# Kernel optimization log

Hardware: AMD Instinct MI355X
Metric: run time of the kernel (lower is better)

## Reference

```python
import jax, jax.numpy as jnp
import numpy as np
import math

N_NODES, N_EDGES = 10000, 160000
CS, CZ, CH, NH, PQ, PV = 384, 128, 192, 12, 4, 8
INF, EPS = 100000.0, 1e-8


def setup_inputs() -> dict:
    key = jax.random.key(0)
    ks = iter(jax.random.split(key, 48))

    def rn(shape, scale=1.0):
        return jax.random.normal(next(ks), shape, jnp.float32) * scale

    def lin(din, dout):
        return rn((din, dout), 1.0 / math.sqrt(din)), jnp.zeros((dout,), jnp.float32)

    s = rn((N_NODES, CS))
    z = rn((N_EDGES, CZ))
    edge_index = jax.random.randint(next(ks), (2, N_EDGES), 0, N_NODES)
    # proper random rotations via QR (sign-corrected)
    A = rn((N_NODES, 3, 3))
    Q, R = jnp.linalg.qr(A)
    rots = Q * jnp.sign(jnp.diagonal(R, axis1=-2, axis2=-1))[:, None, :]
    trans = rn((N_NODES, 3), 10.0)
    mask = jnp.ones((N_NODES,), jnp.float32)
    Ww1, bw1 = lin(2 * CS + CZ, CH)
    Ww2, bw2 = lin(CH, CH)
    Ww3, bw3 = lin(CH, NH)
    Wv1, bv1 = lin(CS + CZ, CH)
    Wv2, bv2 = lin(CH, CH)
    Wv3, bv3 = lin(CH, CH)
    Wq, bq = lin(CS, NH * PQ * 3)
    Wkv, bkv = lin(CS, NH * (PQ + PV) * 3)
    Wb, bb = lin(CZ, NH)
    Wdz, bdz = lin(CZ, CZ // 4)
    Wo, bo = lin(NH * (CZ // 4 + CH // NH + PV * 4), CS)
    hw = jnp.full((NH,), math.log(math.e - 1.0), jnp.float32)  # softplus^-1(1)
    return dict(s=s, z=z, edge_index=edge_index, rots=rots, trans=trans, mask=mask,
                Ww1=Ww1, bw1=bw1, Ww2=Ww2, bw2=bw2, Ww3=Ww3, bw3=bw3,
                Wv1=Wv1, bv1=bv1, Wv2=Wv2, bv2=bv2, Wv3=Wv3, bv3=bv3,
                Wq=Wq, bq=bq, Wkv=Wkv, bkv=bkv, Wb=Wb, bb=bb,
                Wdz=Wdz, bdz=bdz, Wo=Wo, bo=bo, hw=hw)


def _points(flat, rots, t, P):
    # flat [N, 3P] is coord-major (split into 3 chunks then stacked last): p[n, p, c] = flat[n, c*P + p]
    p = flat.reshape(flat.shape[0], 3, P).transpose(0, 2, 1)
    return jnp.einsum('nij,npj->npi', rots, p) + t[:, None, :]


def _forward(s, z, edge_index, rots, trans, mask,
             Ww1, bw1, Ww2, bw2, Ww3, bw3,
             Wv1, bv1, Wv2, bv2, Wv3, bv3,
             Wq, bq, Wkv, bkv, Wb, bb, Wdz, bdz, Wo, bo, hw):
    n = s.shape[0]
    src = edge_index[1]
    dst = edge_index[0]
    t = trans * 0.1  # r.scale_translation(1/10)
    q_pts = _points(s @ Wq + bq, rots, t, NH * PQ).reshape(n, NH, PQ, 3)
    kv_pts = _points(s @ Wkv + bkv, rots, t, NH * (PQ + PV)).reshape(n, NH, PQ + PV, 3)
    k_pts, v_pts = kv_pts[:, :, :PQ], kv_pts[:, :, PQ:]
    b = z @ Wb + bb  # [E, NH]
    w_ins = jnp.concatenate([s[src], s[dst], z], axis=-1)  # [E, 2*CS+CZ]
    h = jax.nn.relu(w_ins @ Ww1 + bw1)
    h = jax.nn.relu(h @ Ww2 + bw2)
    a = (h @ Ww3 + bw3) * math.sqrt(1.0 / (3 * CH)) + math.sqrt(1.0 / 3) * b
    disp = q_pts[src] - k_pts[dst]  # [E, NH, PQ, 3]
    pt_att = jnp.sum(disp ** 2, axis=-1)  # [E, NH, PQ]
    hw_sp = jax.nn.softplus(hw)[None, :, None] * math.sqrt(1.0 / (3 * (PQ * 9.0 / 2)))
    pt_att = jnp.sum(pt_att * hw_sp, axis=-1) * (-0.5)  # [E, NH]
    edge_mask = INF * (mask[dst] * mask[src] - 1.0)
    a = a + pt_att + edge_mask[:, None]
    # segment softmax grouped by edge_index[1]
    amax = jax.ops.segment_max(a, src, num_segments=n)
    ex = jnp.exp(a - amax[src])
    denom = jax.ops.segment_sum(ex, src, num_segments=n)
    a = ex / (denom[src] + 1e-16)
    v_in = jnp.concatenate([s[dst], z], axis=-1)
    h = jax.nn.relu(v_in @ Wv1 + bv1)
    h = jax.nn.relu(h @ Wv2 + bv2)
    v_dst = (h @ Wv3 + bv3).reshape(-1, NH, CH // NH)
    o = jax.ops.segment_sum(a[..., None] * v_dst, src, num_segments=n).reshape(n, -1)
    o_pt = jax.ops.segment_sum(a[..., None, None] * v_pts[dst], src, num_segments=n)  # [n, NH, PV, 3]
    o_pt = jnp.einsum('nji,nhpj->nhpi', rots, o_pt - t[:, None, None, :])  # invert_apply: R^T (x - t)
    o_pt_norm = jnp.sqrt(jnp.sum(o_pt ** 2, axis=-1) + EPS).reshape(n, -1)
    o_pt_flat = o_pt.reshape(n, NH * PV, 3)
    pair_z = z @ Wdz + bdz  # [E, CZ//4]
    o_pair = jax.ops.segment_sum(a[..., None] * pair_z[:, None, :], src, num_segments=n).reshape(n, -1)
    feats = jnp.concatenate([o, o_pt_flat[..., 0], o_pt_flat[..., 1], o_pt_flat[..., 2], o_pt_norm, o_pair], axis=-1)
    return feats @ Wo + bo


def reference(s, z, edge_index, rots, trans, mask,
              Ww1, bw1, Ww2, bw2, Ww3, bw3,
              Wv1, bv1, Wv2, bv2, Wv3, bv3,
              Wq, bq, Wkv, bkv, Wb, bb, Wdz, bdz, Wo, bo, hw):
    return _forward(s, z, edge_index, rots, trans, mask,
                    Ww1, bw1, Ww2, bw2, Ww3, bw3,
                    Wv1, bv1, Wv2, bv2, Wv3, bv3,
                    Wq, bq, Wkv, bkv, Wb, bb, Wdz, bdz, Wo, bo, hw)
```

## Files before the change

kernel.cpp:

```cpp
#include <hip/hip_runtime.h>
#include <hip/hip_bf16.h>
#include <math.h>

#define N_NODES 10000
#define N_EDGES 160000
#define CS 384
#define CZ 128
#define CH 192
#define NH 12
#define PQ 4
#define PV 8

typedef __hip_bfloat16 bf16;
typedef unsigned short ushort;
typedef __attribute__((ext_vector_type(8))) short short8;
typedef __attribute__((ext_vector_type(4))) short s16x4;
typedef __attribute__((ext_vector_type(4))) float f32x4;

__device__ __forceinline__ ushort cvt1(float f) {
  bf16 h = __float2bfloat16(f);
  return __builtin_bit_cast(unsigned short, h);
}
__device__ __forceinline__ short8 lda8f(const float* p, int idx) {
  const f32x4* q = (const f32x4*)(p + idx);
  f32x4 a = q[0], b = q[1];
  short8 r;
  r[0] = (short)cvt1(a[0]); r[1] = (short)cvt1(a[1]);
  r[2] = (short)cvt1(a[2]); r[3] = (short)cvt1(a[3]);
  r[4] = (short)cvt1(b[0]); r[5] = (short)cvt1(b[1]);
  r[6] = (short)cvt1(b[2]); r[7] = (short)cvt1(b[3]);
  return r;
}
__device__ __forceinline__ float bf(ushort u) {
  return __bfloat162float(__builtin_bit_cast(bf16, u));
}

#define OFF_QPTS   0
#define OFF_KPTS   (OFF_QPTS + N_NODES*72)
#define OFF_VPTSH  (OFF_KPTS + N_NODES*72)
#define OFF_SB     (OFF_VPTSH + N_NODES*144)
#define OFF_LOGIT  (OFF_SB + N_NODES*192)
#define OFF_AMAX   (OFF_LOGIT + N_EDGES*12)
#define OFF_DENOM  (OFF_AMAX + N_NODES*12)
#define OFF_ACCO   (OFF_DENOM + N_NODES*12)
#define OFF_ACCP   (OFF_ACCO + N_NODES*192)
#define OFF_ACCZ   (OFF_ACCP + N_NODES*288)
#define FP32_TOTAL (OFF_ACCZ + N_NODES*384)

#define SP_SRC_US  0
#define SP_DST_US  (N_NODES*192)

#define WW1S 0
#define WW2S 172032
#define WW3S 208896
#define WBS  211968
#define WV1S 214016
#define WV2S 312320
#define WV3S 349184
#define WDZS 386048
#define WQS  390144
#define WKVS 445440
#define WOS  611328
#define SWZ_TOTAL 979968

#define IHIST   0
#define ICUR    10000
#define IROWPTR 20000
#define IPERM   30016

__global__ void k_init(float* __restrict__ ws, int* __restrict__ ib) {
  int idx = blockIdx.x * blockDim.x + threadIdx.x;
  const int ntot = N_NODES * (192 + 288);
  if (idx < ntot) ws[OFF_ACCO + idx] = 0.0f;
  if (idx < N_NODES) ib[IHIST + idx] = 0;
}

__global__ void k_zero_accz(float* __restrict__ ws) {
  int idx = blockIdx.x * blockDim.x + threadIdx.x;
  if (idx < N_NODES*384) ws[OFF_ACCZ + idx] = 0.0f;
}

__global__ void k_cast_s(const float* __restrict__ s, ushort* __restrict__ sb) {
  int i = (blockIdx.x * 256 + threadIdx.x) * 4;
  if (i + 3 < N_NODES*CS) {
    f32x4 v = *(const f32x4*)(s + i);
    sb[i]   = cvt1(v[0]); sb[i+1] = cvt1(v[1]);
    sb[i+2] = cvt1(v[2]); sb[i+3] = cvt1(v[3]);
  }
}

struct SwzArgs {
  const float* src[11];
  int off[11], start[11], Nreal[11], NT[11];
};
__global__ void k_swz_all(SwzArgs A, ushort* __restrict__ dst, int grand) {
  int tid = blockIdx.x * blockDim.x + threadIdx.x;
  if (tid >= grand) return;
  int m = 0;
  while (m < 10 && tid >= A.start[m+1]) ++m;
  int t = tid - A.start[m];
  int j = t & 7, lane = (t >> 3) & 63, t2 = t >> 9;
  int nt = t2 % A.NT[m], kt = t2 / A.NT[m];
  int k = kt*32 + (lane >> 4)*8 + j;
  int n = nt*16 + (lane & 15);
  dst[A.off[m] + t] = (n < A.Nreal[m]) ? cvt1(A.src[m][k*A.Nreal[m] + n]) : (ushort)0;
}

__global__ void k_hist(const int* __restrict__ ei, int* __restrict__ ib) {
  int e = blockIdx.x * 256 + threadIdx.x;
  if (e < N_EDGES) atomicAdd(&ib[IHIST + ei[N_EDGES + e]], 1);
}

__global__ __launch_bounds__(1024) void k_scan(int* __restrict__ ib) {
  __shared__ int csum[1024];
  int t = threadIdx.x;
  const int CHUNK = (N_NODES + 1023) / 1024;
  int beg = t * CHUNK;
  int end = beg + CHUNK; if (end > N_NODES) end = N_NODES;
  int s = 0;
  for (int i = beg; i < end && i < N_NODES; ++i) s += ib[IHIST + i];
  csum[t] = s;
  __syncthreads();
  for (int off = 1; off < 1024; off <<= 1) {
    int v = (t >= off) ? csum[t - off] : 0;
    __syncthreads();
    csum[t] += v;
    __syncthreads();
  }
  int run = (t == 0) ? 0 : csum[t - 1];
  for (int i = beg; i < end && i < N_NODES; ++i) {
    ib[IROWPTR + i] = run;
    ib[ICUR + i] = run;
    run += ib[IHIST + i];
  }
  if (t == 1023) ib[IROWPTR + N_NODES] = run;
}

__global__ void k_scatter(const int* __restrict__ ei, int* __restrict__ ib) {
  int e = blockIdx.x * 256 + threadIdx.x;
  if (e < N_EDGES) {
    int pos = atomicAdd(&ib[ICUR + ei[N_EDGES + e]], 1);
    ib[IPERM + pos] = e;
  }
}

__global__ __launch_bounds__(256) void k_sp(
    const ushort* __restrict__ sb, const ushort* __restrict__ wswz,
    ushort* __restrict__ sp) {
  const int n0 = blockIdx.x * 32;
  const int tid = threadIdx.x;
  const int wave = tid >> 6, lane = tid & 63, quad = lane >> 4, l16 = lane & 15;
  const int rowhalf = wave & 1, part = wave >> 1;
  const int row = rowhalf*16 + l16;
  int nd = n0 + row;
  const int nclamp = (nd < N_NODES) ? nd : 0;
  f32x4 acc[12];
#pragma unroll
  for (int i = 0; i < 12; ++i) acc[i] = (f32x4){0.f, 0.f, 0.f, 0.f};
  const short8* bw = (const short8*)(wswz + WW1S);
#pragma unroll 2
  for (int kt = 0; kt < 12; ++kt) {
    short8 av = *(const short8*)(sb + nclamp*384 + kt*32 + quad*8);
    const short8* bk = bw + ((part*12 + kt)*12*64 + lane);
#pragma unroll
    for (int nt = 0; nt < 12; ++nt) {
      short8 bv = bk[nt*64];
      acc[nt] = __builtin_amdgcn_mfma_f32_16x16x32_bf16(av, bv, acc[nt], 0, 0, 0);
    }
  }
  ushort* dst = sp + (part ? SP_DST_US : SP_SRC_US);
#pragma unroll
  for (int nt = 0; nt < 12; ++nt) {
    int col = nt*16 + l16;
#pragma unroll
    for (int r = 0; r < 4; ++r) {
      int node = n0 + rowhalf*16 + quad*4 + r;
      if (node < N_NODES) dst[node*192 + col] = cvt1(acc[nt][r]);
    }
  }
}

__global__ __launch_bounds__(256) void k_node_proj_mfma(
    const ushort* __restrict__ sb, const float* __restrict__ rots, const float* __restrict__ trans,
    const ushort* __restrict__ wswz,
    const float* __restrict__ bq, const float* __restrict__ bkv,
    float* __restrict__ ws) {
  const int n0 = blockIdx.x * 32;
  const int tid = threadIdx.x;
  const int wave = tid >> 6, lane = tid & 63, quad = lane >> 4, l16 = lane & 15;
  const int rowhalf = wave & 1, thalf = wave >> 1;
  __shared__ __align__(16) bf16 pbuf[32][584];
  __shared__ float RmL[32][9], tvL[32][3];
  for (int i = tid; i < 32*9; i += 256) {
    int nl = i/9, j = i - nl*9; int nd = n0 + nl;
    RmL[nl][j] = (nd < N_NODES) ? rots[nd*9 + j] : 0.f;
  }
  for (int i = tid; i < 32*3; i += 256) {
    int nl = i/3, j = i - nl*3; int nd = n0 + nl;
    tvL[nl][j] = (nd < N_NODES) ? 0.1f * trans[nd*3 + j] : 0.f;
  }

  const int row = rowhalf*16 + l16;
  int nd = n0 + row;
  const int nclamp = (nd < N_NODES) ? nd : 0;
  f32x4 acc[18];
#pragma unroll
  for (int i = 0; i < 18; ++i) acc[i] = (f32x4){0.f, 0.f, 0.f, 0.f};
  const short8* bq8 = (const short8*)(wswz + WQS);
  const short8* bkv8 = (const short8*)(wswz + WKVS);
#pragma unroll 2
  for (int kt = 0; kt < 12; ++kt) {
    short8 av = *(const short8*)(sb + nclamp*384 + kt*32 + quad*8);
#pragma unroll
    for (int nt = 0; nt < 18; ++nt) {
      int g = thalf*18 + nt;
      short8 bv = (g < 9) ? bq8[(kt*9 + g)*64 + lane]
                          : bkv8[(kt*27 + (g - 9))*64 + lane];
      acc[nt] = __builtin_amdgcn_mfma_f32_16x16x32_bf16(av, bv, acc[nt], 0, 0, 0);
    }
  }
#pragma unroll
  for (int nt = 0; nt < 18; ++nt) {
    int gcol = (thalf*18 + nt)*16 + l16;
    float bias = (gcol < 144) ? bq[gcol] : bkv[gcol - 144];
#pragma unroll
    for (int r = 0; r < 4; ++r)
      pbuf[rowhalf*16 + quad*4 + r][gcol] = __float2bfloat16(acc[nt][r] + bias);
  }
  __syncthreads();

  bf16* qpb = (bf16*)(ws + OFF_QPTS);
  bf16* kpb = (bf16*)(ws + OFF_KPTS);
  bf16* vph = (bf16*)(ws + OFF_VPTSH);
  for (int i = tid; i < 32*192; i += 256) {
    int nl = i / 192, p = i - nl*192;
    int node = n0 + nl;
    if (node >= N_NODES) continue;
    float c0, c1, c2;
    if (p < 48) {
      c0 = __bfloat162float(pbuf[nl][p]);
      c1 = __bfloat162float(pbuf[nl][48 + p]);
      c2 = __bfloat162float(pbuf[nl][96 + p]);
    } else {
      int q = p - 48;
      c0 = __bfloat162float(pbuf[nl][144 + q]);
      c1 = __bfloat162float(pbuf[nl][288 + q]);
      c2 = __bfloat162float(pbuf[nl][432 + q]);
    }
    const float* Rm = RmL[nl];
    const float* tv = tvL[nl];
    float r0 = Rm[0]*c0 + Rm[1]*c1 + Rm[2]*c2 + tv[0];
    float r1 = Rm[3]*c0 + Rm[4]*c1 + Rm[5]*c2 + tv[1];
    float r2 = Rm[6]*c0 + Rm[7]*c1 + Rm[8]*c2 + tv[2];
    if (p < 48) {
      int base = node*144 + p*3;
      qpb[base]   = __float2bfloat16(r0);
      qpb[base+1] = __float2bfloat16(r1);
      qpb[base+2] = __float2bfloat16(r2);
    } else {
      int q = p - 48; int h = q / 12, idx = q % 12;
      if (idx < PQ) {
        int base = node*144 + (h*PQ + idx)*3;
        kpb[base]   = __float2bfloat16(r0);
        kpb[base+1] = __float2bfloat16(r1);
        kpb[base+2] = __float2bfloat16(r2);
      } else {
        int base = node*288 + (h*PV + (idx - PQ))*3;
        vph[base]   = __float2bfloat16(r0);
        vph[base+1] = __float2bfloat16(r1);
        vph[base+2] = __float2bfloat16(r2);
      }
    }
  }
}

__global__ __launch_bounds__(256) void k_edge_logit_mfma(
    const ushort* __restrict__ sb, const float* __restrict__ zp, const int* __restrict__ ei,
    const float* __restrict__ mask,
    const ushort* __restrict__ wswz,
    const float* __restrict__ bw1, const float* __restrict__ bw2, const float* __restrict__ bw3,
    const float* __restrict__ bb, const float* __restrict__ hw,
    const ushort* __restrict__ qpb, const ushort* __restrict__ kpb,
    const ushort* __restrict__ sps, const ushort* __restrict__ spd,
    const int* __restrict__ ib,
    float* __restrict__ logit) {
  const int e0 = blockIdx.x * 64;
  const int tid = threadIdx.x;
  const int wave = tid >> 6, lane = tid & 63, quad = lane >> 4, l16 = lane & 15;
  __shared__ __align__(16) bf16 hbuf[64][200];
  __shared__ int seL[64], deL[64], eIdL[64];
  if (tid < 64) {
    int e = ib[IPERM + e0 + tid];
    eIdL[tid] = e; deL[tid] = ei[e]; seL[tid] = ei[N_EDGES + e];
  }
  __syncthreads();

  const int r0 = wave*16 + l16;
  const int ez0 = eIdL[r0];

  f32x4 acc0[12];
#pragma unroll
  for (int i = 0; i < 12; ++i) acc0[i] = (f32x4){0.f, 0.f, 0.f, 0.f};
  f32x4 accB0 = (f32x4){0.f, 0.f, 0.f, 0.f};
  const short8* bw = (const short8*)(wswz + WW1S);
  const short8* bB8 = (const short8*)(wswz + WBS);
#pragma unroll 2
  for (int kt = 0; kt < 4; ++kt) {
    int k0 = kt*32 + quad*8;
    short8 a0 = lda8f(zp, ez0*128 + k0);
    const short8* bk = bw + ((24 + kt)*12*64 + lane);
#pragma unroll
    for (int nt = 0; nt < 12; ++nt) {
      short8 bv = bk[nt*64];
      acc0[nt] = __builtin_amdgcn_mfma_f32_16x16x32_bf16(a0, bv, acc0[nt], 0, 0, 0);
    }
    short8 bvB = bB8[kt*64 + lane];
    accB0 = __builtin_amdgcn_mfma_f32_16x16x32_bf16(a0, bvB, accB0, 0, 0, 0);
  }
#pragma unroll
  for (int nt = 0; nt < 12; ++nt) {
    int col = nt*16 + l16;
    float bcol = bw1[col];
#pragma unroll
    for (int r = 0; r < 4; ++r) {
      int row = wave*16 + quad*4 + r;
      float v = acc0[nt][r] + bcol
              + bf(sps[seL[row]*192 + col])
              + bf(spd[deL[row]*192 + col]);
      hbuf[row][col] = __float2bfloat16(fmaxf(v, 0.f));
    }
  }

#pragma unroll
  for (int i = 0; i < 12; ++i) acc0[i] = (f32x4){0.f, 0.f, 0.f, 0.f};
  bw = (const short8*)(wswz + WW2S);
#pragma unroll
  for (int kt = 0; kt < 6; ++kt) {
    short8 a0 = *(const short8*)&hbuf[r0][kt*32 + quad*8];
    const short8* bk = bw + (kt*12*64 + lane);
#pragma unroll
    for (int nt = 0; nt < 12; ++nt) {
      short8 bv = bk[nt*64];
      acc0[nt] = __builtin_amdgcn_mfma_f32_16x16x32_bf16(a0, bv, acc0[nt], 0, 0, 0);
    }
  }
#pragma unroll
  for (int nt = 0; nt < 12; ++nt) {
    float bcol = bw2[nt*16 + l16];
#pragma unroll
    for (int r = 0; r < 4; ++r)
      hbuf[wave*16 + quad*4 + r][nt*16 + l16] =
          __float2bfloat16(fmaxf(acc0[nt][r] + bcol, 0.f));
  }

  f32x4 accW0 = (f32x4){0.f, 0.f, 0.f, 0.f};
  const short8* b3 = (const short8*)(wswz + WW3S);
#pragma unroll
  for (int kt = 0; kt < 6; ++kt) {
    short8 a0 = *(const short8*)&hbuf[r0][kt*32 + quad*8];
    short8 bv = b3[kt*64 + lane];
    accW0 = __builtin_amdgcn_mfma_f32_16x16x32_bf16(a0, bv, accW0, 0, 0, 0);
  }

  if (l16 < 12) {
    const int h = l16;
    float hv = hw[h];
    float hws = logf(1.0f + expf(hv)) * 0.1360827634879543f;
    float b3c = bw3[h], bbc = bb[h];
#pragma unroll
    for (int r = 0; r < 4; ++r) {
      int eloc = wave*16 + quad*4 + r;
      int se = seL[eloc], de = deL[eloc];
      float v = (accW0[r] + b3c) * 0.041666666666666664f + 0.5773502691896258f * (accB0[r] + bbc);
      int qb = se*144 + h*12;
      int kb = de*144 + h*12;
      float pa = 0.f;
#pragma unroll
      for (int t3 = 0; t3 < 3; ++t3) {
        s16x4 qv = *(const s16x4*)(qpb + qb + t3*4);
        s16x4 kv = *(const s16x4*)(kpb + kb + t3*4);
#pragma unroll
        for (int u = 0; u < 4; ++u) {
          float d = bf((ushort)qv[u]) - bf((ushort)kv[u]);
          pa += d*d;
        }
      }
      v -= 0.5f * hws * pa;
      v += 100000.0f * (mask[de] * mask[se] - 1.0f);
      logit[(e0 + eloc)*12 + h] = v;
    }
  }
}

__global__ void k_softmax(float* __restrict__ a, const int* __restrict__ ib) {
  int t = blockIdx.x * 256 + threadIdx.x;
  if (t >= N_NODES * 12) return;
  int n = t / 12, h = t - n*12;
  int b = ib[IROWPTR + n], e = ib[IROWPTR + n + 1];
  if (b == e) return;
  float m = -3.4e38f;
  for (int j = b; j < e; ++j) m = fmaxf(m, a[j*12 + h]);
  float s = 0.f;
  for (int j = b; j < e; ++j) {
    float ex = expf(a[j*12 + h] - m);
    s += ex;
    a[j*12 + h] = ex;
  }
  float inv = 1.f / (s + 1e-16f);
  for (int j = b; j < e; ++j) a[j*12 + h] *= inv;
}

__global__ __launch_bounds__(256) void k_edge_accum_mfma(
    const ushort* __restrict__ sb, const float* __restrict__ zp, const int* __restrict__ ei,
    const ushort* __restrict__ wswz,
    const float* __restrict__ bv1, const float* __restrict__ bv2, const float* __restrict__ bv3,
    const float* __restrict__ bdz,
    const float* __restrict__ aS,
    const bf16* __restrict__ vph, const int* __restrict__ ib,
    float* __restrict__ acc_o, float* __restrict__ acc_p, float* __restrict__ acc_z) {
  const int p0 = blockIdx.x * 64;
  const int tid = threadIdx.x;
  const int wave = tid >> 6, lane = tid & 63, quad = lane >> 4, l16 = lane & 15;
  __shared__ __align__(16) unsigned char smem[64*193*4];
  __shared__ float awL[64][12];
  __shared__ int seL[64], deL[64], eIdL[64];
  bf16* hb = (bf16*)smem;
  float* stg = (float*)smem;
  if (tid < 64) {
    int e = ib[IPERM + p0 + tid];
    eIdL[tid] = e;
    deL[tid] = ei[e];
    seL[tid] = ei[N_EDGES + e];
  }
  __syncthreads();
  for (int i = tid; i < 64*12; i += 256)
    (&awL[0][0])[i] = aS[p0*12 + i];

  const int arow = wave*16 + l16;
  const int edst = deL[arow];
  const int eid  = eIdL[arow];

  f32x4 acc[12];
#pragma unroll
  for (int i = 0; i < 12; ++i) acc[i] = (f32x4){0.f, 0.f, 0.f, 0.f};
  f32x4 apz[2];
  apz[0] = (f32x4){0.f, 0.f, 0.f, 0.f};
  apz[1] = (f32x4){0.f, 0.f, 0.f, 0.f};
  const short8* bw = (const short8*)(wswz + WV1S);
  const short8* bz = (const short8*)(wswz + WDZS);
#pragma unroll 2
  for (int kt = 0; kt < 12; ++kt) {
    short8 av = *(const short8*)(sb + edst*384 + kt*32 + quad*8);
    const short8* bk = bw + (kt*12*64 + lane);
#pragma unroll
    for (int nt = 0; nt < 12; ++nt) {
      short8 bv = bk[nt*64];
      acc[nt] = __builtin_amdgcn_mfma_f32_16x16x32_bf16(av, bv, acc[nt], 0, 0, 0);
    }
  }
#pragma unroll 2
  for (int kt = 12; kt < 16; ++kt) {
    int kz = (kt - 12)*32 + quad*8;
    short8 av = lda8f(zp, eid*128 + kz);
    const short8* bk = bw + (kt*12*64 + lane);
#pragma unroll
    for (int nt = 0; nt < 12; ++nt) {
      short8 bv = bk[nt*64];
      acc[nt] = __builtin_amdgcn_mfma_f32_16x16x32_bf16(av, bv, acc[nt], 0, 0, 0);
    }
#pragma unroll
    for (int nt = 0; nt < 2; ++nt) {
      short8 bvz = bz[((kt - 12)*2 + nt)*64 + lane];
      apz[nt] = __builtin_amdgcn_mfma_f32_16x16x32_bf16(av, bvz, apz[nt], 0, 0, 0);
    }
  }
#pragma unroll
  for (int nt = 0; nt < 12; ++nt) {
    float bcol = bv1[nt*16 + l16];
#pragma unroll
    for (int r = 0; r < 4; ++r)
      hb[(wave*16 + quad*4 + r)*200 + nt*16 + l16] =
          __float2bfloat16(fmaxf(acc[nt][r] + bcol, 0.f));
  }

#pragma unroll
  for (int i = 0; i < 12; ++i) acc[i] = (f32x4){0.f, 0.f, 0.f, 0.f};
  bw = (const short8*)(wswz + WV2S);
#pragma unroll
  for (int kt = 0; kt < 6; ++kt) {
    short8 av = *(const short8*)&hb[(wave*16 + l16)*200 + kt*32 + quad*8];
    const short8* bk = bw + (kt*12*64 + lane);
#pragma unroll
    for (int nt = 0; nt < 12; ++nt) {
      short8 bv = bk[nt*64];
      acc[nt] = __builtin_amdgcn_mfma_f32_16x16x32_bf16(av, bv, acc[nt], 0, 0, 0);
    }
  }
#pragma unroll
  for (int nt = 0; nt < 12; ++nt) {
    float bcol = bv2[nt*16 + l16];
#pragma unroll
    for (int r = 0; r < 4; ++r)
      hb[(wave*16 + quad*4 + r)*200 + nt*16 + l16] =
          __float2bfloat16(fmaxf(acc[nt][r] + bcol, 0.f));
  }

#pragma unroll
  for (int i = 0; i < 12; ++i) acc[i] = (f32x4){0.f, 0.f, 0.f, 0.f};
  bw = (const short8*)(wswz + WV3S);
#pragma unroll
  for (int kt = 0; kt < 6; ++kt) {
    short8 av = *(const short8*)&hb[(wave*16 + l16)*200 + kt*32 + quad*8];
    const short8* bk = bw + (kt*12*64 + lane);
#pragma unroll
    for (int nt = 0; nt < 12; ++nt) {
      short8 bv = bk[nt*64];
      acc[nt] = __builtin_amdgcn_mfma_f32_16x16x32_bf16(av, bv, acc[nt], 0, 0, 0);
    }
  }
  __syncthreads();

#pragma unroll
  for (int nt = 0; nt < 12; ++nt) {
    int col = nt*16 + l16;
    float bcol = bv3[col];
#pragma unroll
    for (int r = 0; r < 4; ++r) {
      int eloc = wave*16 + quad*4 + r;
      stg[eloc*193 + col] = awL[eloc][nt] * (acc[nt][r] + bcol);
    }
  }
  __syncthreads();
  for (int c = tid; c < 192; c += 256) {
    float sum = 0.f;
    for (int r = 0; r < 64; ++r) {
      sum += stg[r*193 + c];
      if (r == 63 || seL[r+1] != seL[r]) {
        atomicAdd(&acc_o[seL[r]*192 + c], sum);
        sum = 0.f;
      }
    }
  }
  __syncthreads();

#pragma unroll
  for (int nt = 0; nt < 2; ++nt) {
    int c = nt*16 + l16;
    float bcol = bdz[c];
#pragma unroll
    for (int r = 0; r < 4; ++r) {
      int eloc = wave*16 + quad*4 + r;
      stg[eloc*33 + c] = apz[nt][r] + bcol;
    }
  }
  __syncthreads();
  for (int p = tid; p < 384; p += 256) {
    int h = p >> 5, c = p & 31;
    float sum = 0.f;
    for (int r = 0; r < 64; ++r) {
      sum += awL[r][h] * stg[r*33 + c];
      if (r == 63 || seL[r+1] != seL[r]) {
        atomicAdd(&acc_z[seL[r]*384 + h*32 + c], sum);
        sum = 0.f;
      }
    }
  }
  __syncthreads();

  for (int ch = 0; ch < 2; ++ch) {
    for (int i = tid; i < 64*144; i += 256) {
      int eloc = i / 144, jj = i - eloc*144;
      int j = ch*144 + jj;
      int h = j / 24;
      stg[eloc*145 + jj] = awL[eloc][h] * __bfloat162float(vph[deL[eloc]*288 + j]);
    }
    __syncthreads();
    for (int c = tid; c < 144; c += 256) {
      float sum = 0.f;
      for (int r = 0; r < 64; ++r) {
        sum += stg[r*145 + c];
        if (r == 63 || seL[r+1] != seL[r]) {
          atomicAdd(&acc_p[seL[r]*288 + ch*144 + c], sum);
          sum = 0.f;
        }
      }
    }
    __syncthreads();
  }
}

__global__ __launch_bounds__(256) void k_node_out_mfma(
    const float* __restrict__ rots, const float* __restrict__ trans,
    const ushort* __restrict__ wswz, const float* __restrict__ bo,
    const float* __restrict__ acc_o, const float* __restrict__ acc_p,
    const float* __restrict__ acc_z, float* __restrict__ out) {
  const int n0 = blockIdx.x * 32;
  const int tid = threadIdx.x;
  const int wave = tid >> 6, lane = tid & 63, quad = lane >> 4, l16 = lane & 15;
  __shared__ __align__(16) bf16 fbuf[32][968];
  __shared__ float RmL[32][9], tvL[32][3];
  for (int i = tid; i < 32*9; i += 256) {
    int nl = i/9, j = i - nl*9; int nd = n0 + nl;
    RmL[nl][j] = (nd < N_NODES) ? rots[nd*9 + j] : 0.f;
  }
  for (int i = tid; i < 32*3; i += 256) {
    int nl = i/3, j = i - nl*3; int nd = n0 + nl;
    tvL[nl][j] = (nd < N_NODES) ? 0.1f * trans[nd*3 + j] : 0.f;
  }
  __syncthreads();
  for (int i = tid; i < 32*192; i += 256) {
    int nl = i/192, c = i - nl*192; int nd = n0 + nl;
    fbuf[nl][c] = __float2bfloat16((nd < N_NODES) ? acc_o[nd*192 + c] : 0.f);
  }
  for (int i = tid; i < 32*96; i += 256) {
    int nl = i/96, pt = i - nl*96; int nd = n0 + nl;
    float r0 = 0.f, r1 = 0.f, r2 = 0.f, nm = 0.f;
    if (nd < N_NODES) {
      const float* Rm = RmL[nl];
      float v0 = acc_p[nd*288 + pt*3 + 0] - tvL[nl][0];
      float v1 = acc_p[nd*288 + pt*3 + 1] - tvL[nl][1];
      float v2 = acc_p[nd*288 + pt*3 + 2] - tvL[nl][2];
      r0 = Rm[0]*v0 + Rm[3]*v1 + Rm[6]*v2;
      r1 = Rm[1]*v0 + Rm[4]*v1 + Rm[7]*v2;
      r2 = Rm[2]*v0 + Rm[5]*v1 + Rm[8]*v2;
      nm = sqrtf(r0*r0 + r1*r1 + r2*r2 + 1e-8f);
    }
    fbuf[nl][192 + pt] = __float2bfloat16(r0);
    fbuf[nl][288 + pt] = __float2bfloat16(r1);
    fbuf[nl][384 + pt] = __float2bfloat16(r2);
    fbuf[nl][480 + pt] = __float2bfloat16(nm);
  }
  for (int i = tid; i < 32*384; i += 256) {
    int nl = i/384, c = i - nl*384; int nd = n0 + nl;
    fbuf[nl][576 + c] = __float2bfloat16((nd < N_NODES) ? acc_z[nd*384 + c] : 0.f);
  }
  __syncthreads();

  const int rowhalf = wave & 1, thalf = wave >> 1;
  f32x4 acc[12];
#pragma unroll
  for (int i = 0; i < 12; ++i) acc[i] = (f32x4){0.f, 0.f, 0.f, 0.f};
  const short8* bwo = (const short8*)(wswz + WOS);
#pragma unroll 2
  for (int kt = 0; kt < 30; ++kt) {
    short8 av = *(const short8*)&fbuf[rowhalf*16 + l16][kt*32 + quad*8];
#pragma unroll
    for (int nt = 0; nt < 12; ++nt) {
      short8 bv = bwo[(kt*24 + thalf*12 + nt)*64 + lane];
      acc[nt] = __builtin_amdgcn_mfma_f32_16x16x32_bf16(av, bv, acc[nt], 0, 0, 0);
    }
  }
#pragma unroll
  for (int nt = 0; nt < 12; ++nt) {
    int col = (thalf*12 + nt)*16 + l16;
    float bias = bo[col];
#pragma unroll
    for (int r = 0; r < 4; ++r) {
      int nd = n0 + rowhalf*16 + quad*4 + r;
      if (nd < N_NODES) out[nd*384 + col] = acc[nt][r] + bias;
    }
  }
}

extern "C" void kernel_launch(void* const* d_in, const int* in_sizes, int n_in,
                              void* d_out, int out_size, void* d_ws, size_t ws_size,
                              hipStream_t stream) {
  const float* s     = (const float*)d_in[0];
  const float* z     = (const float*)d_in[1];
  const int*   ei    = (const int*)d_in[2];
  const float* rots  = (const float*)d_in[3];
  const float* trans = (const float*)d_in[4];
  const float* mask  = (const float*)d_in[5];
  const float* Ww1 = (const float*)d_in[6];  const float* bw1 = (const float*)d_in[7];
  const float* Ww2 = (const float*)d_in[8];  const float* bw2 = (const float*)d_in[9];
  const float* Ww3 = (const float*)d_in[10]; const float* bw3 = (const float*)d_in[11];
  const float* Wv1 = (const float*)d_in[12]; const float* bv1 = (const float*)d_in[13];
  const float* Wv2 = (const float*)d_in[14]; const float* bv2 = (const float*)d_in[15];
  const float* Wv3 = (const float*)d_in[16]; const float* bv3 = (const float*)d_in[17];
  const float* Wq  = (const float*)d_in[18]; const float* bq  = (const float*)d_in[19];
  const float* Wkv = (const float*)d_in[20]; const float* bkv = (const float*)d_in[21];
  const float* Wb  = (const float*)d_in[22]; const float* bb  = (const float*)d_in[23];
  const float* Wdz = (const float*)d_in[24]; const float* bdz = (const float*)d_in[25];
  const float* Wo  = (const float*)d_in[26]; const float* bo  = (const float*)d_in[27];
  const float* hw  = (const float*)d_in[28];
  float* ws = (float*)d_ws;
  ushort* wswz = (ushort*)(ws + FP32_TOTAL);
  int* ib = (int*)(wswz + SWZ_TOTAL);
  float* out = (float*)d_out;
  ushort* sb = (ushort*)(ws + OFF_SB);
  ushort* sp = (ushort*)(ws + OFF_ACCZ);

  const int ntot = N_NODES * (192 + 288);
  k_init<<<(ntot + 255)/256, 256, 0, stream>>>(ws, ib);
  k_cast_s<<<(N_NODES*CS/4 + 255)/256, 256, 0, stream>>>(s, sb);

  SwzArgs A;
  const float* srcs[11] = {Ww1, Ww2, Ww3, Wb, Wv1, Wv2, Wv3, Wdz, Wq, Wkv, Wo};
  int offs[11]   = {WW1S, WW2S, WW3S, WBS, WV1S, WV2S, WV3S, WDZS, WQS, WKVS, WOS};
  int Ks[11]     = {896, 192, 192, 128, 512, 192, 192, 128, 384, 384, 960};
  int Nreals[11] = {192, 192, 12, 12, 192, 192, 192, 32, 144, 432, 384};
  int NTs[11]    = {12, 12, 1, 1, 12, 12, 12, 2, 9, 27, 24};
  int cum = 0;
  for (int m = 0; m < 11; ++m) {
    A.src[m] = srcs[m]; A.off[m] = offs[m]; A.start[m] = cum;
    A.Nreal[m] = Nreals[m]; A.NT[m] = NTs[m];
    cum += (Ks[m]/32) * NTs[m] * 512;
  }
  k_swz_all<<<(cum + 255)/256, 256, 0, stream>>>(A, wswz, cum);

  k_hist<<<(N_EDGES + 255)/256, 256, 0, stream>>>(ei, ib);
  k_scan<<<1, 1024, 0, stream>>>(ib);
  k_scatter<<<(N_EDGES + 255)/256, 256, 0, stream>>>(ei, ib);

  k_node_proj_mfma<<<(N_NODES + 31)/32, 256, 0, stream>>>(
      sb, rots, trans, wswz, bq, bkv, ws);

  k_sp<<<(N_NODES + 31)/32, 256, 0, stream>>>(sb, wswz, sp);

  k_edge_logit_mfma<<<N_EDGES/64, 256, 0, stream>>>(
      sb, z, ei, mask, wswz,
      bw1, bw2, bw3, bb, hw,
      (const ushort*)(ws + OFF_QPTS), (const ushort*)(ws + OFF_KPTS),
      sp + SP_SRC_US, sp + SP_DST_US,
      ib, ws + OFF_LOGIT);

  k_zero_accz<<<(N_NODES*384 + 255)/256, 256, 0, stream>>>(ws);

  k_softmax<<<(N_NODES*12 + 255)/256, 256, 0, stream>>>(ws + OFF_LOGIT, ib);

  k_edge_accum_mfma<<<N_EDGES/64, 256, 0, stream>>>(
      sb, z, ei, wswz,
      bv1, bv2, bv3, bdz,
      ws + OFF_LOGIT,
      (const bf16*)(ws + OFF_VPTSH), ib,
      ws + OFF_ACCO, ws + OFF_ACCP, ws + OFF_ACCZ);

  k_node_out_mfma<<<(N_NODES + 31)/32, 256, 0, stream>>>(
      rots, trans, wswz, bo,
      ws + OFF_ACCO, ws + OFF_ACCP, ws + OFF_ACCZ, out);
}
```

Before: 785.0 us.

## Precompute per-node s@Wv1 projection instead of recomputing per edge

The s-part of the first value-MLP layer depends only on the destination node, so a new kernel computes s@Wv1[:384] once per node into a bf16 buffer. The edge accumulation kernel then skips the 12 K-tiles of MFMA over gathered s rows and adds the gathered precomputed row in the bias/ReLU epilogue. This cuts per-edge matmul work by about three quarters for that layer. The cost is an extra kernel, an extra bf16 rounding of the partial sum, and reuse of the QPTS workspace region, which must not be needed after the logit kernel.

New measurement: 774.9 us. About the same (-1.3%).

```diff
diff --git a/kernel.cpp b/kernel.cpp
--- a/kernel.cpp
+++ b/kernel.cpp
@@ -176,6 +176,40 @@
     for (int r = 0; r < 4; ++r) {
       int node = n0 + rowhalf*16 + quad*4 + r;
       if (node < N_NODES) dst[node*192 + col] = cvt1(acc[nt][r]);
+    }
+  }
+}
+
+__global__ __launch_bounds__(256) void k_sv(
+    const ushort* __restrict__ sb, const ushort* __restrict__ wswz,
+    ushort* __restrict__ sv) {
+  const int n0 = blockIdx.x * 64;
+  const int tid = threadIdx.x;
+  const int wave = tid >> 6, lane = tid & 63, quad = lane >> 4, l16 = lane & 15;
+  const int row = wave*16 + l16;
+  int nd = n0 + row;
+  const int nclamp = (nd < N_NODES) ? nd : 0;
+  f32x4 acc[12];
+#pragma unroll
+  for (int i = 0; i < 12; ++i) acc[i] = (f32x4){0.f, 0.f, 0.f, 0.f};
+  const short8* bw = (const short8*)(wswz + WV1S);
+#pragma unroll 2
+  for (int kt = 0; kt < 12; ++kt) {
+    short8 av = *(const short8*)(sb + nclamp*384 + kt*32 + quad*8);
+    const short8* bk = bw + (kt*12*64 + lane);
+#pragma unroll
+    for (int nt = 0; nt < 12; ++nt) {
+      short8 bv = bk[nt*64];
+      acc[nt] = __builtin_amdgcn_mfma_f32_16x16x32_bf16(av, bv, acc[nt], 0, 0, 0);
+    }
+  }
+#pragma unroll
+  for (int nt = 0; nt < 12; ++nt) {
+    int col = nt*16 + l16;
+#pragma unroll
+    for (int r = 0; r < 4; ++r) {
+      int node = n0 + wave*16 + quad*4 + r;
+      if (node < N_NODES) sv[node*192 + col] = cvt1(acc[nt][r]);
     }
   }
 }
@@ -411,11 +445,12 @@
 }
 
 __global__ __launch_bounds__(256) void k_edge_accum_mfma(
-    const ushort* __restrict__ sb, const float* __restrict__ zp, const int* __restrict__ ei,
+    const float* __restrict__ zp, const int* __restrict__ ei,
     const ushort* __restrict__ wswz,
     const float* __restrict__ bv1, const float* __restrict__ bv2, const float* __restrict__ bv3,
     const float* __restrict__ bdz,
     const float* __restrict__ aS,
+    const ushort* __restrict__ sv,
     const bf16* __restrict__ vph, const int* __restrict__ ib,
     float* __restrict__ acc_o, float* __restrict__ acc_p, float* __restrict__ acc_z) {
   const int p0 = blockIdx.x * 64;
@@ -437,7 +472,6 @@
     (&awL[0][0])[i] = aS[p0*12 + i];
 
   const int arow = wave*16 + l16;
-  const int edst = deL[arow];
   const int eid  = eIdL[arow];
 
   f32x4 acc[12];
@@ -449,16 +483,6 @@
   const short8* bw = (const short8*)(wswz + WV1S);
   const short8* bz = (const short8*)(wswz + WDZS);
 #pragma unroll 2
-  for (int kt = 0; kt < 12; ++kt) {
-    short8 av = *(const short8*)(sb + edst*384 + kt*32 + quad*8);
-    const short8* bk = bw + (kt*12*64 + lane);
-#pragma unroll
-    for (int nt = 0; nt < 12; ++nt) {
-      short8 bv = bk[nt*64];
-      acc[nt] = __builtin_amdgcn_mfma_f32_16x16x32_bf16(av, bv, acc[nt], 0, 0, 0);
-    }
-  }
-#pragma unroll 2
   for (int kt = 12; kt < 16; ++kt) {
     int kz = (kt - 12)*32 + quad*8;
     short8 av = lda8f(zp, eid*128 + kz);
@@ -476,11 +500,14 @@
   }
 #pragma unroll
   for (int nt = 0; nt < 12; ++nt) {
-    float bcol = bv1[nt*16 + l16];
-#pragma unroll
-    for (int r = 0; r < 4; ++r)
-      hb[(wave*16 + quad*4 + r)*200 + nt*16 + l16] =
-          __float2bfloat16(fmaxf(acc[nt][r] + bcol, 0.f));
+    int col = nt*16 + l16;
+    float bcol = bv1[col];
+#pragma unroll
+    for (int r = 0; r < 4; ++r) {
+      int eloc = wave*16 + quad*4 + r;
+      float v = acc[nt][r] + bcol + bf(sv[deL[eloc]*192 + col]);
+      hb[eloc*200 + col] = __float2bfloat16(fmaxf(v, 0.f));
+    }
   }
 
 #pragma unroll
@@ -689,6 +716,7 @@
   float* out = (float*)d_out;
   ushort* sb = (ushort*)(ws + OFF_SB);
   ushort* sp = (ushort*)(ws + OFF_ACCZ);
+  ushort* sv = (ushort*)(ws + OFF_QPTS);
 
   const int ntot = N_NODES * (192 + 288);
   k_init<<<(ntot + 255)/256, 256, 0, stream>>>(ws, ib);
@@ -724,14 +752,16 @@
       sp + SP_SRC_US, sp + SP_DST_US,
       ib, ws + OFF_LOGIT);
 
+  k_sv<<<(N_NODES + 63)/64, 256, 0, stream>>>(sb, wswz, sv);
   k_zero_accz<<<(N_NODES*384 + 255)/256, 256, 0, stream>>>(ws);
 
   k_softmax<<<(N_NODES*12 + 255)/256, 256, 0, stream>>>(ws + OFF_LOGIT, ib);
 
   k_edge_accum_mfma<<<N_EDGES/64, 256, 0, stream>>>(
-      sb, z, ei, wswz,
+      z, ei, wswz,
       bv1, bv2, bv3, bdz,
       ws + OFF_LOGIT,
+      sv,
       (const bf16*)(ws + OFF_VPTSH), ib,
       ws + OFF_ACCO, ws + OFF_ACCP, ws + OFF_ACCZ);
 
```
